# Optimization experiments

Hardware: AMD Instinct MI355X
Metric: run time of the kernel (lower is better)

The kernel has to match this reference:

```python
import jax, jax.numpy as jnp
import numpy as np

N = 8388608
HID = 8
P = 10.0
EPS = 1e-8
LR = 1.0
EXP_P = float(np.exp(np.float32(P)))  # exp(10) ~ 22026.466


def setup_inputs() -> dict:
    key = jax.random.key(0)
    ks = jax.random.split(key, 12)
    s = 0.3
    inp = {
        "h": jnp.zeros((N, HID), jnp.float32),
        "g": jax.random.normal(ks[0], (N,), jnp.float32),
        # GRUCell params (flax: input denses no bias, hidden denses with bias)
        "Wi_r": jax.random.normal(ks[1], (2, HID), jnp.float32) * s,
        "Wh_r": jax.random.normal(ks[2], (HID, HID), jnp.float32) * s,
        "bh_r": jax.random.normal(ks[3], (HID,), jnp.float32) * s,
        "Wi_z": jax.random.normal(ks[4], (2, HID), jnp.float32) * s,
        "Wh_z": jax.random.normal(ks[5], (HID, HID), jnp.float32) * s,
        "bh_z": jax.random.normal(ks[6], (HID,), jnp.float32) * s,
        "Wi_n": jax.random.normal(ks[7], (2, HID), jnp.float32) * s,
        "Wh_n": jax.random.normal(ks[8], (HID, HID), jnp.float32) * s,
        "bh_n": jax.random.normal(ks[9], (HID,), jnp.float32) * s,
        # MLP: single Dense(1) (mlp_dims=(), trailing relu popped)
        "Wm": jax.random.normal(ks[10], (HID, 1), jnp.float32) * s,
        "bm": jax.random.normal(ks[11], (1,), jnp.float32) * s,
    }
    return inp


def reference(h, g, Wi_r, Wh_r, bh_r, Wi_z, Wh_z, bh_z, Wi_n, Wh_n, bh_n, Wm, bm):
    g2 = jax.lax.stop_gradient(g[..., None])            # [N,1]
    g_sign = jnp.sign(g2)
    g_log = jnp.log(jnp.abs(g2) + EPS) / P              # [N,1]
    g_in1 = jnp.concatenate([g_log, g_sign], axis=-1)   # [N,2]
    g_in2 = jnp.concatenate([-jnp.ones_like(g2), EXP_P * g2], axis=-1)
    g_in = jnp.where(g_log >= -1.0, g_in1, g_in2)       # [N,2] (broadcast select)

    # flax GRUCell: r,z gates sigmoid, candidate tanh, input dense has no bias
    r = jax.nn.sigmoid(g_in @ Wi_r + h @ Wh_r + bh_r)
    z = jax.nn.sigmoid(g_in @ Wi_z + h @ Wh_z + bh_z)
    n = jnp.tanh(g_in @ Wi_n + r * (h @ Wh_n + bh_n))
    h_new = (1.0 - z) * n + z * h                        # [N,8]

    outs = h_new @ Wm + bm                               # [N,1]
    out = -LR * jnp.exp(outs) * g2                       # [N,1]
    return h_new, out[..., 0]
```

## Files before the change

### kernel.cpp

```cpp
#include <hip/hip_runtime.h>


#define SWZ(x, imm) __int_as_float(__builtin_amdgcn_ds_swizzle(__float_as_int(x), (imm)))
#define PIN(x) asm volatile("" : "+v"(x))

__global__ __launch_bounds__(256, 4) void gru_l2l_kernel(
    const float* __restrict__ hp, const float* __restrict__ gp,
    const float* __restrict__ Wi_r, const float* __restrict__ Wh_r, const float* __restrict__ bh_r,
    const float* __restrict__ Wi_z, const float* __restrict__ Wh_z, const float* __restrict__ bh_z,
    const float* __restrict__ Wi_n, const float* __restrict__ Wh_n, const float* __restrict__ bh_n,
    const float* __restrict__ Wm, const float* __restrict__ bm,
    float* __restrict__ out, int nrows)
{
    const int tot    = nrows << 3;
    const int tid    = blockIdx.x * blockDim.x + threadIdx.x;
    const int stride = blockDim.x * gridDim.x;
    const int j      = tid & 7;

    const float L2E = 1.44269504088896341f;

    float wir0 = Wi_r[j] * L2E, wir1 = Wi_r[8 + j] * L2E;
    float wiz0 = Wi_z[j] * L2E, wiz1 = Wi_z[8 + j] * L2E;
    float win0 = Wi_n[j],       win1 = Wi_n[8 + j];
    float whr[8], whz[8], whn[8];
#pragma unroll
    for (int k = 0; k < 8; ++k) {
        whr[k] = Wh_r[k * 8 + j] * L2E;
        whz[k] = Wh_z[k * 8 + j] * L2E;
        whn[k] = Wh_n[k * 8 + j];
    }
    float br = bh_r[j] * L2E, bz = bh_z[j] * L2E, bn = bh_n[j];
    float wm   = Wm[j];
    float bmv2 = bm[0] * L2E;

    PIN(wir0); PIN(wir1); PIN(wiz0); PIN(wiz1); PIN(win0); PIN(win1);
#pragma unroll
    for (int k = 0; k < 8; ++k) { PIN(whr[k]); PIN(whz[k]); PIN(whn[k]); }
    PIN(br); PIN(bz); PIN(bn); PIN(wm); PIN(bmv2);
    asm volatile("" ::: "memory");

    float* __restrict__ outo = out + tot;

    for (int i = tid; i < tot; i += stride) {
        const int   row  = i >> 3;
        const float hval = hp[i];
        const float g    = gp[row];

        const float ag = fabsf(g) + 1e-8f;
        const float lg = __builtin_amdgcn_logf(ag) * 0.069314718055994531f;
        float gin0, gin1;
        if (lg >= -1.0f) {
            gin0 = lg;
            gin1 = (g > 0.0f) ? 1.0f : -1.0f;
        } else {
            gin0 = -1.0f;
            gin1 = 22026.465794806718f * g;
        }

        const float hk0 = SWZ(hval, 0x018), hk1 = SWZ(hval, 0x038);
        const float hk2 = SWZ(hval, 0x058), hk3 = SWZ(hval, 0x078);
        const float hk4 = SWZ(hval, 0x098), hk5 = SWZ(hval, 0x0B8);
        const float hk6 = SWZ(hval, 0x0D8), hk7 = SWZ(hval, 0x0F8);

        float ar = fmaf(gin0, wir0, fmaf(gin1, wir1, br));
        float az = fmaf(gin0, wiz0, fmaf(gin1, wiz1, bz));
        float an = fmaf(gin0, win0, gin1 * win1);
        float hn = bn;
#define DOT3(K) \
        ar = fmaf(hk##K, whr[K], ar); \
        az = fmaf(hk##K, whz[K], az); \
        hn = fmaf(hk##K, whn[K], hn);
        DOT3(0) DOT3(1) DOT3(2) DOT3(3) DOT3(4) DOT3(5) DOT3(6) DOT3(7)
#undef DOT3

        const float r = __builtin_amdgcn_rcpf(1.0f + __builtin_amdgcn_exp2f(-ar));
        const float z = __builtin_amdgcn_rcpf(1.0f + __builtin_amdgcn_exp2f(-az));
        const float pre = fmaf(r, hn, an);
        const float t    = __builtin_amdgcn_exp2f(-2.885390081777927f * fabsf(pre));
        const float nval = copysignf((1.0f - t) * __builtin_amdgcn_rcpf(1.0f + t), pre);
        const float hnew = fmaf(z, hval - nval, nval);
        out[i] = hnew;

        float s = hnew * wm;
        s += SWZ(s, 0x041F);
        s += SWZ(s, 0x081F);
        s += SWZ(s, 0x101F);
        if (j == 0) {
            outo[row] = -__builtin_amdgcn_exp2f(fmaf(s, L2E, bmv2)) * g;
        }
    }
}

extern "C" void kernel_launch(void* const* d_in, const int* in_sizes, int n_in,
                              void* d_out, int out_size, void* d_ws, size_t ws_size,
                              hipStream_t stream) {
    const float* hp   = (const float*)d_in[0];
    const float* gp   = (const float*)d_in[1];
    const float* Wi_r = (const float*)d_in[2];
    const float* Wh_r = (const float*)d_in[3];
    const float* bh_r = (const float*)d_in[4];
    const float* Wi_z = (const float*)d_in[5];
    const float* Wh_z = (const float*)d_in[6];
    const float* bh_z = (const float*)d_in[7];
    const float* Wi_n = (const float*)d_in[8];
    const float* Wh_n = (const float*)d_in[9];
    const float* bh_n = (const float*)d_in[10];
    const float* Wm   = (const float*)d_in[11];
    const float* bm   = (const float*)d_in[12];
    const int nrows   = in_sizes[1];

    gru_l2l_kernel<<<8192, 256, 0, stream>>>(hp, gp, Wi_r, Wh_r, bh_r,
                                             Wi_z, Wh_z, bh_z,
                                             Wi_n, Wh_n, bh_n,
                                             Wm, bm, (float*)d_out, nrows);
}
```

Measured before the change: 551.5 us.

## Process two hidden units per thread with packed FP32 FMAs and float2 loads

```diff
diff --git a/kernel.cpp b/kernel.cpp
--- a/kernel.cpp
+++ b/kernel.cpp
@@ -1,8 +1,23 @@
 #include <hip/hip_runtime.h>
 
 
+typedef float f32x2 __attribute__((ext_vector_type(2)));
+
 #define SWZ(x, imm) __int_as_float(__builtin_amdgcn_ds_swizzle(__float_as_int(x), (imm)))
 #define PIN(x) asm volatile("" : "+v"(x))
+
+#define PK_FMA_BLO(d, a, bp) \
+    asm("v_pk_fma_f32 %0, %1, %2, %0 op_sel:[0,0,0] op_sel_hi:[1,0,1]" \
+        : "+v"(d) : "v"(a), "v"(bp))
+#define PK_FMA_BHI(d, a, bp) \
+    asm("v_pk_fma_f32 %0, %1, %2, %0 op_sel:[0,1,0] op_sel_hi:[1,1,1]" \
+        : "+v"(d) : "v"(a), "v"(bp))
+#define PK_FMA3_BLO(d, a, bp, c) \
+    asm("v_pk_fma_f32 %0, %1, %2, %3 op_sel:[0,0,0] op_sel_hi:[1,0,1]" \
+        : "=v"(d) : "v"(a), "v"(bp), "v"(c))
+#define PK_MUL_BLO(d, a, bp) \
+    asm("v_pk_mul_f32 %0, %1, %2 op_sel:[0,0] op_sel_hi:[1,0]" \
+        : "=v"(d) : "v"(a), "v"(bp))
 
 __global__ __launch_bounds__(256, 4) void gru_l2l_kernel(
     const float* __restrict__ hp, const float* __restrict__ gp,
@@ -12,80 +27,108 @@
     const float* __restrict__ Wm, const float* __restrict__ bm,
     float* __restrict__ out, int nrows)
 {
-    const int tot    = nrows << 3;
+    const int npairs = nrows << 2;
     const int tid    = blockIdx.x * blockDim.x + threadIdx.x;
     const int stride = blockDim.x * gridDim.x;
-    const int j      = tid & 7;
+    const int m      = tid & 3;
+    const int c0     = m << 1;
 
     const float L2E = 1.44269504088896341f;
 
-    float wir0 = Wi_r[j] * L2E, wir1 = Wi_r[8 + j] * L2E;
-    float wiz0 = Wi_z[j] * L2E, wiz1 = Wi_z[8 + j] * L2E;
-    float win0 = Wi_n[j],       win1 = Wi_n[8 + j];
-    float whr[8], whz[8], whn[8];
+    f32x2 wir0 = { Wi_r[c0] * L2E,     Wi_r[c0 + 1] * L2E };
+    f32x2 wir1 = { Wi_r[8 + c0] * L2E, Wi_r[8 + c0 + 1] * L2E };
+    f32x2 wiz0 = { Wi_z[c0] * L2E,     Wi_z[c0 + 1] * L2E };
+    f32x2 wiz1 = { Wi_z[8 + c0] * L2E, Wi_z[8 + c0 + 1] * L2E };
+    f32x2 win0 = { Wi_n[c0],           Wi_n[c0 + 1] };
+    f32x2 win1 = { Wi_n[8 + c0],       Wi_n[8 + c0 + 1] };
+    f32x2 whr[8], whz[8], whn[8];
 #pragma unroll
     for (int k = 0; k < 8; ++k) {
-        whr[k] = Wh_r[k * 8 + j] * L2E;
-        whz[k] = Wh_z[k * 8 + j] * L2E;
-        whn[k] = Wh_n[k * 8 + j];
+        whr[k] = (f32x2){ Wh_r[k * 8 + c0] * L2E, Wh_r[k * 8 + c0 + 1] * L2E };
+        whz[k] = (f32x2){ Wh_z[k * 8 + c0] * L2E, Wh_z[k * 8 + c0 + 1] * L2E };
+        whn[k] = (f32x2){ Wh_n[k * 8 + c0],       Wh_n[k * 8 + c0 + 1] };
     }
-    float br = bh_r[j] * L2E, bz = bh_z[j] * L2E, bn = bh_n[j];
-    float wm   = Wm[j];
+    f32x2 br = { bh_r[c0] * L2E, bh_r[c0 + 1] * L2E };
+    f32x2 bz = { bh_z[c0] * L2E, bh_z[c0 + 1] * L2E };
+    f32x2 bn = { bh_n[c0],       bh_n[c0 + 1] };
+    float wmx  = Wm[c0], wmy = Wm[c0 + 1];
     float bmv2 = bm[0] * L2E;
 
     PIN(wir0); PIN(wir1); PIN(wiz0); PIN(wiz1); PIN(win0); PIN(win1);
 #pragma unroll
     for (int k = 0; k < 8; ++k) { PIN(whr[k]); PIN(whz[k]); PIN(whn[k]); }
-    PIN(br); PIN(bz); PIN(bn); PIN(wm); PIN(bmv2);
+    PIN(br); PIN(bz); PIN(bn); PIN(wmx); PIN(wmy); PIN(bmv2);
     asm volatile("" ::: "memory");
 
-    float* __restrict__ outo = out + tot;
+    const f32x2* __restrict__ hp2  = (const f32x2*)hp;
+    f32x2* __restrict__       out2 = (f32x2*)out;
+    float* __restrict__       outo = out + ((long)nrows << 3);
 
-    for (int i = tid; i < tot; i += stride) {
-        const int   row  = i >> 3;
-        const float hval = hp[i];
-        const float g    = gp[row];
+    for (int p = tid; p < npairs; p += stride) {
+        const int   row = p >> 2;
+        f32x2       hv  = hp2[p];
+        const float g   = gp[row];
 
         const float ag = fabsf(g) + 1e-8f;
         const float lg = __builtin_amdgcn_logf(ag) * 0.069314718055994531f;
-        float gin0, gin1;
+        f32x2 gin;
         if (lg >= -1.0f) {
-            gin0 = lg;
-            gin1 = (g > 0.0f) ? 1.0f : -1.0f;
+            gin.x = lg;
+            gin.y = (g > 0.0f) ? 1.0f : -1.0f;
         } else {
-            gin0 = -1.0f;
-            gin1 = 22026.465794806718f * g;
+            gin.x = -1.0f;
+            gin.y = 22026.465794806718f * g;
         }
 
-        const float hk0 = SWZ(hval, 0x018), hk1 = SWZ(hval, 0x038);
-        const float hk2 = SWZ(hval, 0x058), hk3 = SWZ(hval, 0x078);
-        const float hk4 = SWZ(hval, 0x098), hk5 = SWZ(hval, 0x0B8);
-        const float hk6 = SWZ(hval, 0x0D8), hk7 = SWZ(hval, 0x0F8);
+        f32x2 hb0, hb1, hb2, hb3;
+        hb0.x = SWZ(hv.x, 0x01C); hb0.y = SWZ(hv.y, 0x01C);
+        hb1.x = SWZ(hv.x, 0x03C); hb1.y = SWZ(hv.y, 0x03C);
+        hb2.x = SWZ(hv.x, 0x05C); hb2.y = SWZ(hv.y, 0x05C);
+        hb3.x = SWZ(hv.x, 0x07C); hb3.y = SWZ(hv.y, 0x07C);
 
-        float ar = fmaf(gin0, wir0, fmaf(gin1, wir1, br));
-        float az = fmaf(gin0, wiz0, fmaf(gin1, wiz1, bz));
-        float an = fmaf(gin0, win0, gin1 * win1);
-        float hn = bn;
-#define DOT3(K) \
-        ar = fmaf(hk##K, whr[K], ar); \
-        az = fmaf(hk##K, whz[K], az); \
-        hn = fmaf(hk##K, whn[K], hn);
-        DOT3(0) DOT3(1) DOT3(2) DOT3(3) DOT3(4) DOT3(5) DOT3(6) DOT3(7)
-#undef DOT3
+        f32x2 ar, az, an, hn;
+        PK_FMA3_BLO(ar, wir0, gin, br);
+        PK_FMA_BHI (ar, wir1, gin);
+        PK_FMA3_BLO(az, wiz0, gin, bz);
+        PK_FMA_BHI (az, wiz1, gin);
+        PK_MUL_BLO (an, win0, gin);
+        PK_FMA_BHI (an, win1, gin);
+        PK_FMA3_BLO(hn, whn[0], hb0, bn);
+        PK_FMA_BLO (ar, whr[0], hb0);
+        PK_FMA_BLO (az, whz[0], hb0);
+        PK_FMA_BHI (ar, whr[1], hb0);
+        PK_FMA_BHI (az, whz[1], hb0);
+        PK_FMA_BHI (hn, whn[1], hb0);
+#define DOT2(Q, K0, K1) \
+        PK_FMA_BLO(ar, whr[K0], hb##Q); \
+        PK_FMA_BLO(az, whz[K0], hb##Q); \
+        PK_FMA_BLO(hn, whn[K0], hb##Q); \
+        PK_FMA_BHI(ar, whr[K1], hb##Q); \
+        PK_FMA_BHI(az, whz[K1], hb##Q); \
+        PK_FMA_BHI(hn, whn[K1], hb##Q);
+        DOT2(1, 2, 3) DOT2(2, 4, 5) DOT2(3, 6, 7)
+#undef DOT2
 
-        const float r = __builtin_amdgcn_rcpf(1.0f + __builtin_amdgcn_exp2f(-ar));
-        const float z = __builtin_amdgcn_rcpf(1.0f + __builtin_amdgcn_exp2f(-az));
-        const float pre = fmaf(r, hn, an);
-        const float t    = __builtin_amdgcn_exp2f(-2.885390081777927f * fabsf(pre));
-        const float nval = copysignf((1.0f - t) * __builtin_amdgcn_rcpf(1.0f + t), pre);
-        const float hnew = fmaf(z, hval - nval, nval);
-        out[i] = hnew;
+        const float rx = __builtin_amdgcn_rcpf(1.0f + __builtin_amdgcn_exp2f(-ar.x));
+        const float ry = __builtin_amdgcn_rcpf(1.0f + __builtin_amdgcn_exp2f(-ar.y));
+        const float zx = __builtin_amdgcn_rcpf(1.0f + __builtin_amdgcn_exp2f(-az.x));
+        const float zy = __builtin_amdgcn_rcpf(1.0f + __builtin_amdgcn_exp2f(-az.y));
 
-        float s = hnew * wm;
+        const float prex = fmaf(rx, hn.x, an.x);
+        const float prey = fmaf(ry, hn.y, an.y);
+        const float tx = __builtin_amdgcn_exp2f(-2.885390081777927f * fabsf(prex));
+        const float ty = __builtin_amdgcn_exp2f(-2.885390081777927f * fabsf(prey));
+        const float nx = copysignf((1.0f - tx) * __builtin_amdgcn_rcpf(1.0f + tx), prex);
+        const float ny = copysignf((1.0f - ty) * __builtin_amdgcn_rcpf(1.0f + ty), prey);
+        const float hnx = fmaf(zx, hv.x - nx, nx);
+        const float hny = fmaf(zy, hv.y - ny, ny);
+        f32x2 ho; ho.x = hnx; ho.y = hny;
+        out2[p] = ho;
+
+        float s = fmaf(hny, wmy, hnx * wmx);
         s += SWZ(s, 0x041F);
         s += SWZ(s, 0x081F);
-        s += SWZ(s, 0x101F);
-        if (j == 0) {
+        if (m == 0) {
             outo[row] = -__builtin_amdgcn_exp2f(fmaf(s, L2E, bmv2)) * g;
         }
     }
```

Result: slower. 566.8 us (+2.8%).

## Process two rows per thread with packed FP32 FMAs and software prefetch

Applied to the files above, without the earlier changes.

```diff
diff --git a/kernel.cpp b/kernel.cpp
--- a/kernel.cpp
+++ b/kernel.cpp
@@ -1,10 +1,32 @@
 #include <hip/hip_runtime.h>
 
+
+typedef float f32x2 __attribute__((ext_vector_type(2)));
 
 #define SWZ(x, imm) __int_as_float(__builtin_amdgcn_ds_swizzle(__float_as_int(x), (imm)))
 #define PIN(x) asm volatile("" : "+v"(x))
 
-__global__ __launch_bounds__(256, 4) void gru_l2l_kernel(
+#define PK_FMA_WLO(d, wp, x) \
+    asm("v_pk_fma_f32 %0, %1, %2, %0 op_sel:[0,0,0] op_sel_hi:[0,1,1]" \
+        : "+v"(d) : "v"(wp), "v"(x))
+#define PK_FMA_WHI(d, wp, x) \
+    asm("v_pk_fma_f32 %0, %1, %2, %0 op_sel:[1,0,0] op_sel_hi:[1,1,1]" \
+        : "+v"(d) : "v"(wp), "v"(x))
+#define PK_FMA3_WLO_CLO(d, wp, x, cp) \
+    asm("v_pk_fma_f32 %0, %1, %2, %3 op_sel:[0,0,0] op_sel_hi:[0,1,0]" \
+        : "=v"(d) : "v"(wp), "v"(x), "v"(cp))
+#define PK_FMA3_WLO_CHI(d, wp, x, cp) \
+    asm("v_pk_fma_f32 %0, %1, %2, %3 op_sel:[0,0,1] op_sel_hi:[0,1,1]" \
+        : "=v"(d) : "v"(wp), "v"(x), "v"(cp))
+#define PK_MUL_WLO(d, wp, x) \
+    asm("v_pk_mul_f32 %0, %1, %2 op_sel:[0,0] op_sel_hi:[0,1]" \
+        : "=v"(d) : "v"(wp), "v"(x))
+#define PK_MUL_WHI(d, wp, x) \
+    asm("v_pk_mul_f32 %0, %1, %2 op_sel:[1,0] op_sel_hi:[1,1]" \
+        : "=v"(d) : "v"(wp), "v"(x))
+
+__global__ __launch_bounds__(256) __attribute__((amdgpu_waves_per_eu(4, 5)))
+void gru_l2l_kernel(
     const float* __restrict__ hp, const float* __restrict__ gp,
     const float* __restrict__ Wi_r, const float* __restrict__ Wh_r, const float* __restrict__ bh_r,
     const float* __restrict__ Wi_z, const float* __restrict__ Wh_z, const float* __restrict__ bh_z,
@@ -12,82 +34,143 @@
     const float* __restrict__ Wm, const float* __restrict__ bm,
     float* __restrict__ out, int nrows)
 {
-    const int tot    = nrows << 3;
-    const int tid    = blockIdx.x * blockDim.x + threadIdx.x;
-    const int stride = blockDim.x * gridDim.x;
-    const int j      = tid & 7;
+    const int NP    = nrows >> 1;
+    const int tid   = blockIdx.x * blockDim.x + threadIdx.x;
+    const int qstep = (blockDim.x * gridDim.x) >> 3;
+    const int j     = tid & 7;
 
     const float L2E = 1.44269504088896341f;
 
-    float wir0 = Wi_r[j] * L2E, wir1 = Wi_r[8 + j] * L2E;
-    float wiz0 = Wi_z[j] * L2E, wiz1 = Wi_z[8 + j] * L2E;
-    float win0 = Wi_n[j],       win1 = Wi_n[8 + j];
-    float whr[8], whz[8], whn[8];
+    f32x2 wirp = { Wi_r[j] * L2E, Wi_r[8 + j] * L2E };
+    f32x2 wizp = { Wi_z[j] * L2E, Wi_z[8 + j] * L2E };
+    f32x2 winp = { Wi_n[j],       Wi_n[8 + j] };
+    f32x2 whrp[4], whzp[4], whnp[4];
 #pragma unroll
-    for (int k = 0; k < 8; ++k) {
-        whr[k] = Wh_r[k * 8 + j] * L2E;
-        whz[k] = Wh_z[k * 8 + j] * L2E;
-        whn[k] = Wh_n[k * 8 + j];
+    for (int k = 0; k < 4; ++k) {
+        whrp[k] = (f32x2){ Wh_r[(2*k)*8 + j] * L2E, Wh_r[(2*k+1)*8 + j] * L2E };
+        whzp[k] = (f32x2){ Wh_z[(2*k)*8 + j] * L2E, Wh_z[(2*k+1)*8 + j] * L2E };
+        whnp[k] = (f32x2){ Wh_n[(2*k)*8 + j],       Wh_n[(2*k+1)*8 + j] };
     }
-    float br = bh_r[j] * L2E, bz = bh_z[j] * L2E, bn = bh_n[j];
-    float wm   = Wm[j];
-    float bmv2 = bm[0] * L2E;
+    f32x2 brzp  = { bh_r[j] * L2E, bh_z[j] * L2E };
+    f32x2 bnwmp = { bh_n[j],       Wm[j] };
+    float bmv2  = bm[0] * L2E;
 
-    PIN(wir0); PIN(wir1); PIN(wiz0); PIN(wiz1); PIN(win0); PIN(win1);
+    PIN(wirp); PIN(wizp); PIN(winp);
 #pragma unroll
-    for (int k = 0; k < 8; ++k) { PIN(whr[k]); PIN(whz[k]); PIN(whn[k]); }
-    PIN(br); PIN(bz); PIN(bn); PIN(wm); PIN(bmv2);
+    for (int k = 0; k < 4; ++k) { PIN(whrp[k]); PIN(whzp[k]); PIN(whnp[k]); }
+    PIN(brzp); PIN(bnwmp); PIN(bmv2);
     asm volatile("" ::: "memory");
 
-    float* __restrict__ outo = out + tot;
+    float* __restrict__ outo = out + ((long)nrows << 3);
 
-    for (int i = tid; i < tot; i += stride) {
-        const int   row  = i >> 3;
-        const float hval = hp[i];
-        const float g    = gp[row];
+    auto doPair = [&](const int q, const f32x2 g2, const float hvA, const float hvB,
+                      const bool dual) {
+        const float gA = g2.x, gB = g2.y;
+        const float agA = fabsf(gA) + 1e-8f;
+        const float agB = fabsf(gB) + 1e-8f;
+        const float lgA = __builtin_amdgcn_logf(agA) * 0.069314718055994531f;
+        const float lgB = __builtin_amdgcn_logf(agB) * 0.069314718055994531f;
+        const bool hiA = (lgA >= -1.0f), hiB = (lgB >= -1.0f);
+        f32x2 gin0p, gin1p;
+        gin0p.x = hiA ? lgA : -1.0f;
+        gin0p.y = hiB ? lgB : -1.0f;
+        gin1p.x = hiA ? ((gA > 0.0f) ? 1.0f : -1.0f) : 22026.465794806718f * gA;
+        gin1p.y = hiB ? ((gB > 0.0f) ? 1.0f : -1.0f) : 22026.465794806718f * gB;
 
-        const float ag = fabsf(g) + 1e-8f;
-        const float lg = __builtin_amdgcn_logf(ag) * 0.069314718055994531f;
-        float gin0, gin1;
-        if (lg >= -1.0f) {
-            gin0 = lg;
-            gin1 = (g > 0.0f) ? 1.0f : -1.0f;
+        f32x2 hb0, hb1, hb2, hb3, hb4, hb5, hb6, hb7;
+        hb0.x = SWZ(hvA, 0x018); hb0.y = SWZ(hvB, 0x018);
+        hb1.x = SWZ(hvA, 0x038); hb1.y = SWZ(hvB, 0x038);
+        hb2.x = SWZ(hvA, 0x058); hb2.y = SWZ(hvB, 0x058);
+        hb3.x = SWZ(hvA, 0x078); hb3.y = SWZ(hvB, 0x078);
+        hb4.x = SWZ(hvA, 0x098); hb4.y = SWZ(hvB, 0x098);
+        hb5.x = SWZ(hvA, 0x0B8); hb5.y = SWZ(hvB, 0x0B8);
+        hb6.x = SWZ(hvA, 0x0D8); hb6.y = SWZ(hvB, 0x0D8);
+        hb7.x = SWZ(hvA, 0x0F8); hb7.y = SWZ(hvB, 0x0F8);
+
+        f32x2 ar2, az2, an2, hn2;
+        PK_FMA3_WLO_CLO(ar2, wirp, gin0p, brzp);
+        PK_FMA_WHI     (ar2, wirp, gin1p);
+        PK_FMA3_WLO_CHI(az2, wizp, gin0p, brzp);
+        PK_FMA_WHI     (az2, wizp, gin1p);
+        PK_MUL_WLO     (an2, winp, gin0p);
+        PK_FMA_WHI     (an2, winp, gin1p);
+        PK_FMA3_WLO_CLO(hn2, whnp[0], hb0, bnwmp);
+        PK_FMA_WLO     (ar2, whrp[0], hb0);
+        PK_FMA_WLO     (az2, whzp[0], hb0);
+        PK_FMA_WHI     (ar2, whrp[0], hb1);
+        PK_FMA_WHI     (az2, whzp[0], hb1);
+        PK_FMA_WHI     (hn2, whnp[0], hb1);
+#define DOTP(KP, QA, QB) \
+        PK_FMA_WLO(ar2, whrp[KP], QA); \
+        PK_FMA_WLO(az2, whzp[KP], QA); \
+        PK_FMA_WLO(hn2, whnp[KP], QA); \
+        PK_FMA_WHI(ar2, whrp[KP], QB); \
+        PK_FMA_WHI(az2, whzp[KP], QB); \
+        PK_FMA_WHI(hn2, whnp[KP], QB);
+        DOTP(1, hb2, hb3) DOTP(2, hb4, hb5) DOTP(3, hb6, hb7)
+#undef DOTP
+
+        const float rA = __builtin_amdgcn_rcpf(1.0f + __builtin_amdgcn_exp2f(-ar2.x));
+        const float rB = __builtin_amdgcn_rcpf(1.0f + __builtin_amdgcn_exp2f(-ar2.y));
+        const float zA = __builtin_amdgcn_rcpf(1.0f + __builtin_amdgcn_exp2f(-az2.x));
+        const float zB = __builtin_amdgcn_rcpf(1.0f + __builtin_amdgcn_exp2f(-az2.y));
+
+        const float preA = fmaf(rA, hn2.x, an2.x);
+        const float preB = fmaf(rB, hn2.y, an2.y);
+        const float tA = __builtin_amdgcn_exp2f(-2.885390081777927f * fabsf(preA));
+        const float tB = __builtin_amdgcn_exp2f(-2.885390081777927f * fabsf(preB));
+        const float nA = copysignf((1.0f - tA) * __builtin_amdgcn_rcpf(1.0f + tA), preA);
+        const float nB = copysignf((1.0f - tB) * __builtin_amdgcn_rcpf(1.0f + tB), preB);
+        const float hnA = fmaf(zA, hvA - nA, nA);
+        const float hnB = fmaf(zB, hvB - nB, nB);
+
+        out[(long)q * 16 + j] = hnA;
+        if (dual) out[(long)q * 16 + 8 + j] = hnB;
+
+        f32x2 hnew2; hnew2.x = hnA; hnew2.y = hnB;
+        f32x2 s2; PK_MUL_WHI(s2, bnwmp, hnew2);
+        s2.x += SWZ(s2.x, 0x041F); s2.y += SWZ(s2.y, 0x041F);
+        s2.x += SWZ(s2.x, 0x081F); s2.y += SWZ(s2.y, 0x081F);
+        s2.x += SWZ(s2.x, 0x101F); s2.y += SWZ(s2.y, 0x101F);
+        const float oA = -__builtin_amdgcn_exp2f(fmaf(s2.x, L2E, bmv2)) * gA;
+        const float oB = -__builtin_amdgcn_exp2f(fmaf(s2.y, L2E, bmv2)) * gB;
+        if (dual) {
+            if (j == 0) {
+                f32x2 o2; o2.x = oA; o2.y = oB;
+                *reinterpret_cast<f32x2*>(outo + 2 * (long)q) = o2;
+            }
         } else {
-            gin0 = -1.0f;
-            gin1 = 22026.465794806718f * g;
+            if (j == 0) outo[2 * (long)q] = oA;
         }
+    };
 
-        const float hk0 = SWZ(hval, 0x018), hk1 = SWZ(hval, 0x038);
-        const float hk2 = SWZ(hval, 0x058), hk3 = SWZ(hval, 0x078);
-        const float hk4 = SWZ(hval, 0x098), hk5 = SWZ(hval, 0x0B8);
-        const float hk6 = SWZ(hval, 0x0D8), hk7 = SWZ(hval, 0x0F8);
+    int q = tid >> 3;
+    if (q < NP) {
+        f32x2 g2  = *reinterpret_cast<const f32x2*>(gp + 2 * (long)q);
+        float hvA = hp[(long)q * 16 + j];
+        float hvB = hp[(long)q * 16 + 8 + j];
+        int qn = q + qstep;
+        for (;;) {
+            const bool more = (qn < NP);
+            f32x2 g2n = g2; float hvAn = hvA, hvBn = hvB;
+            if (more) {
+                g2n  = *reinterpret_cast<const f32x2*>(gp + 2 * (long)qn);
+                hvAn = hp[(long)qn * 16 + j];
+                hvBn = hp[(long)qn * 16 + 8 + j];
+            }
+            doPair(q, g2, hvA, hvB, true);
+            if (!more) break;
+            q = qn; g2 = g2n; hvA = hvAn; hvB = hvBn;
+            qn += qstep;
+        }
+    }
 
-        float ar = fmaf(gin0, wir0, fmaf(gin1, wir1, br));
-        float az = fmaf(gin0, wiz0, fmaf(gin1, wiz1, bz));
-        float an = fmaf(gin0, win0, gin1 * win1);
-        float hn = bn;
-#define DOT3(K) \
-        ar = fmaf(hk##K, whr[K], ar); \
-        az = fmaf(hk##K, whz[K], az); \
-        hn = fmaf(hk##K, whn[K], hn);
-        DOT3(0) DOT3(1) DOT3(2) DOT3(3) DOT3(4) DOT3(5) DOT3(6) DOT3(7)
-#undef DOT3
-
-        const float r = __builtin_amdgcn_rcpf(1.0f + __builtin_amdgcn_exp2f(-ar));
-        const float z = __builtin_amdgcn_rcpf(1.0f + __builtin_amdgcn_exp2f(-az));
-        const float pre = fmaf(r, hn, an);
-        const float t    = __builtin_amdgcn_exp2f(-2.885390081777927f * fabsf(pre));
-        const float nval = copysignf((1.0f - t) * __builtin_amdgcn_rcpf(1.0f + t), pre);
-        const float hnew = fmaf(z, hval - nval, nval);
-        out[i] = hnew;
-
-        float s = hnew * wm;
-        s += SWZ(s, 0x041F);
-        s += SWZ(s, 0x081F);
-        s += SWZ(s, 0x101F);
-        if (j == 0) {
-            outo[row] = -__builtin_amdgcn_exp2f(fmaf(s, L2E, bmv2)) * g;
-        }
+    if ((nrows & 1) && blockIdx.x == 0 && threadIdx.x < 8) {
+        const long r = nrows - 1;
+        const float g  = gp[r];
+        const float hv = hp[r * 8 + j];
+        f32x2 g2t; g2t.x = g; g2t.y = g;
+        doPair((int)(r >> 1), g2t, hv, hv, false);
     }
 }
 
@@ -109,7 +192,7 @@
     const float* bm   = (const float*)d_in[12];
     const int nrows   = in_sizes[1];
 
-    gru_l2l_kernel<<<8192, 256, 0, stream>>>(hp, gp, Wi_r, Wh_r, bh_r,
+    gru_l2l_kernel<<<2048, 256, 0, stream>>>(hp, gp, Wi_r, Wh_r, bh_r,
                                              Wi_z, Wh_z, bh_z,
                                              Wi_n, Wh_n, bh_n,
                                              Wm, bm, (float*)d_out, nrows);
```

Result: no change. 542.0 us (-1.7%).

## Process row pairs with packed FMA and software-pipelined prefetch loop

Applied to the files above, without the earlier changes.

```diff
diff --git a/kernel.cpp b/kernel.cpp
--- a/kernel.cpp
+++ b/kernel.cpp
@@ -1,10 +1,17 @@
 #include <hip/hip_runtime.h>
 
+
+typedef float f32x2 __attribute__((ext_vector_type(2)));
 
 #define SWZ(x, imm) __int_as_float(__builtin_amdgcn_ds_swizzle(__float_as_int(x), (imm)))
 #define PIN(x) asm volatile("" : "+v"(x))
 
-__global__ __launch_bounds__(256, 4) void gru_l2l_kernel(
+static __device__ __forceinline__ f32x2 splat2(float v) { f32x2 r; r.x = v; r.y = v; return r; }
+static __device__ __forceinline__ f32x2 fma2(float w, f32x2 x, f32x2 a) {
+    return __builtin_elementwise_fma(splat2(w), x, a);
+}
+
+__global__ __launch_bounds__(256, 2) void gru_l2l_kernel(
     const float* __restrict__ hp, const float* __restrict__ gp,
     const float* __restrict__ Wi_r, const float* __restrict__ Wh_r, const float* __restrict__ bh_r,
     const float* __restrict__ Wi_z, const float* __restrict__ Wh_z, const float* __restrict__ bh_z,
@@ -12,10 +19,11 @@
     const float* __restrict__ Wm, const float* __restrict__ bm,
     float* __restrict__ out, int nrows)
 {
-    const int tot    = nrows << 3;
-    const int tid    = blockIdx.x * blockDim.x + threadIdx.x;
-    const int stride = blockDim.x * gridDim.x;
-    const int j      = tid & 7;
+    const int NP  = nrows >> 1;
+    const int tid = blockIdx.x * blockDim.x + threadIdx.x;
+    const int st  = (blockDim.x * gridDim.x) >> 3;
+    const int g0  = tid >> 3;
+    const int j   = tid & 7;
 
     const float L2E = 1.44269504088896341f;
 
@@ -30,64 +38,117 @@
         whn[k] = Wh_n[k * 8 + j];
     }
     float br = bh_r[j] * L2E, bz = bh_z[j] * L2E, bn = bh_n[j];
-    float wm   = Wm[j];
+    float wm = Wm[j];
     float bmv2 = bm[0] * L2E;
 
     PIN(wir0); PIN(wir1); PIN(wiz0); PIN(wiz1); PIN(win0); PIN(win1);
 #pragma unroll
     for (int k = 0; k < 8; ++k) { PIN(whr[k]); PIN(whz[k]); PIN(whn[k]); }
     PIN(br); PIN(bz); PIN(bn); PIN(wm); PIN(bmv2);
-    asm volatile("" ::: "memory");
 
-    float* __restrict__ outo = out + tot;
+    float* __restrict__ outo = out + ((long)nrows << 3);
 
-    for (int i = tid; i < tot; i += stride) {
-        const int   row  = i >> 3;
-        const float hval = hp[i];
-        const float g    = gp[row];
+    auto doPair = [&](const float hvA, const float hvB, const f32x2 g2,
+                      const int q, const bool dual) {
+        const float gA = g2.x, gB = g2.y;
+        const float agA = fabsf(gA) + 1e-8f;
+        const float agB = fabsf(gB) + 1e-8f;
+        const float lgA = __builtin_amdgcn_logf(agA) * 0.069314718055994531f;
+        const float lgB = __builtin_amdgcn_logf(agB) * 0.069314718055994531f;
+        const bool hiA = (lgA >= -1.0f), hiB = (lgB >= -1.0f);
+        f32x2 gi0, gi1;
+        gi0.x = hiA ? lgA : -1.0f;
+        gi0.y = hiB ? lgB : -1.0f;
+        gi1.x = hiA ? ((gA > 0.0f) ? 1.0f : -1.0f) : 22026.465794806718f * gA;
+        gi1.y = hiB ? ((gB > 0.0f) ? 1.0f : -1.0f) : 22026.465794806718f * gB;
 
-        const float ag = fabsf(g) + 1e-8f;
-        const float lg = __builtin_amdgcn_logf(ag) * 0.069314718055994531f;
-        float gin0, gin1;
-        if (lg >= -1.0f) {
-            gin0 = lg;
-            gin1 = (g > 0.0f) ? 1.0f : -1.0f;
+        f32x2 hb0, hb1, hb2, hb3, hb4, hb5, hb6, hb7;
+        hb0.x = SWZ(hvA, 0x018); hb0.y = SWZ(hvB, 0x018);
+        hb1.x = SWZ(hvA, 0x038); hb1.y = SWZ(hvB, 0x038);
+        hb2.x = SWZ(hvA, 0x058); hb2.y = SWZ(hvB, 0x058);
+        hb3.x = SWZ(hvA, 0x078); hb3.y = SWZ(hvB, 0x078);
+        hb4.x = SWZ(hvA, 0x098); hb4.y = SWZ(hvB, 0x098);
+        hb5.x = SWZ(hvA, 0x0B8); hb5.y = SWZ(hvB, 0x0B8);
+        hb6.x = SWZ(hvA, 0x0D8); hb6.y = SWZ(hvB, 0x0D8);
+        hb7.x = SWZ(hvA, 0x0F8); hb7.y = SWZ(hvB, 0x0F8);
+
+        f32x2 ar, az, an, hn;
+        ar = fma2(wir1, gi1, fma2(wir0, gi0, splat2(br)));
+        az = fma2(wiz1, gi1, fma2(wiz0, gi0, splat2(bz)));
+        an = fma2(win1, gi1, splat2(win0) * gi0);
+        hn = splat2(bn);
+#define DOTK(K, HB) \
+        ar = fma2(whr[K], HB, ar); \
+        az = fma2(whz[K], HB, az); \
+        hn = fma2(whn[K], HB, hn);
+        DOTK(0, hb0) DOTK(1, hb1) DOTK(2, hb2) DOTK(3, hb3)
+        DOTK(4, hb4) DOTK(5, hb5) DOTK(6, hb6) DOTK(7, hb7)
+#undef DOTK
+
+        const float rA = __builtin_amdgcn_rcpf(1.0f + __builtin_amdgcn_exp2f(-ar.x));
+        const float rB = __builtin_amdgcn_rcpf(1.0f + __builtin_amdgcn_exp2f(-ar.y));
+        const float zA = __builtin_amdgcn_rcpf(1.0f + __builtin_amdgcn_exp2f(-az.x));
+        const float zB = __builtin_amdgcn_rcpf(1.0f + __builtin_amdgcn_exp2f(-az.y));
+
+        const float preA = fmaf(rA, hn.x, an.x);
+        const float preB = fmaf(rB, hn.y, an.y);
+        const float tA = __builtin_amdgcn_exp2f(-2.885390081777927f * fabsf(preA));
+        const float tB = __builtin_amdgcn_exp2f(-2.885390081777927f * fabsf(preB));
+        const float nA = copysignf((1.0f - tA) * __builtin_amdgcn_rcpf(1.0f + tA), preA);
+        const float nB = copysignf((1.0f - tB) * __builtin_amdgcn_rcpf(1.0f + tB), preB);
+        const float hnA = fmaf(zA, hvA - nA, nA);
+        const float hnB = fmaf(zB, hvB - nB, nB);
+
+        out[(long)q * 16 + j] = hnA;
+        if (dual) out[(long)q * 16 + 8 + j] = hnB;
+
+        float sA = hnA * wm, sB = hnB * wm;
+        sA += SWZ(sA, 0x041F); sB += SWZ(sB, 0x041F);
+        sA += SWZ(sA, 0x081F); sB += SWZ(sB, 0x081F);
+        sA += SWZ(sA, 0x101F); sB += SWZ(sB, 0x101F);
+        const float oA = -__builtin_amdgcn_exp2f(fmaf(sA, L2E, bmv2)) * gA;
+        const float oB = -__builtin_amdgcn_exp2f(fmaf(sB, L2E, bmv2)) * gB;
+        if (dual) {
+            if (j == 0) {
+                f32x2 o2; o2.x = oA; o2.y = oB;
+                *reinterpret_cast<f32x2*>(outo + 2 * (long)q) = o2;
+            }
         } else {
-            gin0 = -1.0f;
-            gin1 = 22026.465794806718f * g;
+            if (j == 0) outo[2 * (long)q] = oA;
         }
+    };
 
-        const float hk0 = SWZ(hval, 0x018), hk1 = SWZ(hval, 0x038);
-        const float hk2 = SWZ(hval, 0x058), hk3 = SWZ(hval, 0x078);
-        const float hk4 = SWZ(hval, 0x098), hk5 = SWZ(hval, 0x0B8);
-        const float hk6 = SWZ(hval, 0x0D8), hk7 = SWZ(hval, 0x0F8);
+    float hA0, hA1, hA2, hA3, hB0, hB1, hB2, hB3;
+    f32x2 gg0, gg1, gg2, gg3;
+    const int NPm1 = NP - 1;
+#define LOADS(S, Q) { int qq = (Q); qq = qq > NPm1 ? NPm1 : qq;           \
+        const long b = (long)qq << 4;                                     \
+        hA##S = hp[b + j]; hB##S = hp[b + 8 + j];                         \
+        gg##S = *reinterpret_cast<const f32x2*>(gp + ((long)qq << 1)); }
 
-        float ar = fmaf(gin0, wir0, fmaf(gin1, wir1, br));
-        float az = fmaf(gin0, wiz0, fmaf(gin1, wiz1, bz));
-        float an = fmaf(gin0, win0, gin1 * win1);
-        float hn = bn;
-#define DOT3(K) \
-        ar = fmaf(hk##K, whr[K], ar); \
-        az = fmaf(hk##K, whz[K], az); \
-        hn = fmaf(hk##K, whn[K], hn);
-        DOT3(0) DOT3(1) DOT3(2) DOT3(3) DOT3(4) DOT3(5) DOT3(6) DOT3(7)
-#undef DOT3
+    int qc = g0;
+    if (qc < NP) {
+        LOADS(0, qc) LOADS(1, qc + st) LOADS(2, qc + 2 * st) LOADS(3, qc + 3 * st)
+        int qr = qc + 4 * st;
+        while (qc + 3 * st < NP) {
+            doPair(hA0, hB0, gg0, qc,          true);  LOADS(0, qr)
+            doPair(hA1, hB1, gg1, qc + st,     true);  LOADS(1, qr + st)
+            doPair(hA2, hB2, gg2, qc + 2 * st, true);  LOADS(2, qr + 2 * st)
+            doPair(hA3, hB3, gg3, qc + 3 * st, true);  LOADS(3, qr + 3 * st)
+            qc += st << 2; qr += st << 2;
+        }
+        if (qc < NP)          doPair(hA0, hB0, gg0, qc,          true);
+        if (qc + st < NP)     doPair(hA1, hB1, gg1, qc + st,     true);
+        if (qc + 2 * st < NP) doPair(hA2, hB2, gg2, qc + 2 * st, true);
+    }
+#undef LOADS
 
-        const float r = __builtin_amdgcn_rcpf(1.0f + __builtin_amdgcn_exp2f(-ar));
-        const float z = __builtin_amdgcn_rcpf(1.0f + __builtin_amdgcn_exp2f(-az));
-        const float pre = fmaf(r, hn, an);
-        const float t    = __builtin_amdgcn_exp2f(-2.885390081777927f * fabsf(pre));
-        const float nval = copysignf((1.0f - t) * __builtin_amdgcn_rcpf(1.0f + t), pre);
-        const float hnew = fmaf(z, hval - nval, nval);
-        out[i] = hnew;
-
-        float s = hnew * wm;
-        s += SWZ(s, 0x041F);
-        s += SWZ(s, 0x081F);
-        s += SWZ(s, 0x101F);
-        if (j == 0) {
-            outo[row] = -__builtin_amdgcn_exp2f(fmaf(s, L2E, bmv2)) * g;
-        }
+    if ((nrows & 1) && blockIdx.x == 0 && threadIdx.x < 8) {
+        const long r = nrows - 1;
+        const float g  = gp[r];
+        const float hv = hp[r * 8 + j];
+        f32x2 gt; gt.x = g; gt.y = g;
+        doPair(hv, hv, gt, (int)(r >> 1), false);
     }
 }
 
@@ -109,7 +170,7 @@
     const float* bm   = (const float*)d_in[12];
     const int nrows   = in_sizes[1];
 
-    gru_l2l_kernel<<<8192, 256, 0, stream>>>(hp, gp, Wi_r, Wh_r, bh_r,
+    gru_l2l_kernel<<<2048, 256, 0, stream>>>(hp, gp, Wi_r, Wh_r, bh_r,
                                              Wi_z, Wh_z, bh_z,
                                              Wi_n, Wh_n, bh_n,
                                              Wm, bm, (float*)d_out, nrows);
```

Result: faster. 523.8 us (-5.0%).
